# Optimization experiments

Hardware: AMD Instinct MI355X
Metric: run time of the kernel (lower is better)

## Reference

```python
import jax, jax.numpy as jnp
import numpy as np

N_NODES, N_EDGES, MAX_NB = 40000, 80000, 4
INPUT_SIZE, NODE_FDIM, HIDDEN = 384, 256, 256
DEPTH = 6


def setup_inputs() -> dict:
    key = jax.random.key(0)
    ks = jax.random.split(key, 16)
    s = 0.05  # weight init scale
    return {
        "fnode": jax.random.normal(ks[0], (N_NODES, NODE_FDIM), dtype=jnp.float32),
        "fmess": jax.random.normal(ks[1], (N_EDGES, INPUT_SIZE), dtype=jnp.float32),
        "agraph": jax.random.randint(ks[2], (N_NODES, MAX_NB), 0, N_EDGES),
        "bgraph": jax.random.randint(ks[3], (N_EDGES, MAX_NB), 0, N_EDGES),
        "mask": jnp.ones((N_NODES, 1), dtype=jnp.float32),
        "Wz": jax.random.normal(ks[4], (INPUT_SIZE + HIDDEN, HIDDEN), dtype=jnp.float32) * s,
        "bz": jnp.zeros((HIDDEN,), dtype=jnp.float32),
        "Wr": jax.random.normal(ks[5], (INPUT_SIZE, HIDDEN), dtype=jnp.float32) * s,
        "Ur": jax.random.normal(ks[6], (HIDDEN, HIDDEN), dtype=jnp.float32) * s,
        "bur": jnp.zeros((HIDDEN,), dtype=jnp.float32),
        "Wh": jax.random.normal(ks[7], (INPUT_SIZE + HIDDEN, HIDDEN), dtype=jnp.float32) * s,
        "bh": jnp.zeros((HIDDEN,), dtype=jnp.float32),
        "Wo": jax.random.normal(ks[8], (NODE_FDIM + HIDDEN, HIDDEN), dtype=jnp.float32) * s,
        "bo": jnp.zeros((HIDDEN,), dtype=jnp.float32),
        "depth": DEPTH,
    }


def reference(fnode, fmess, agraph, bgraph, mask, Wz, bz, Wr, Ur, bur, Wh, bh, Wo, bo, depth):
    E, H = fmess.shape[0], Wz.shape[1]
    # message 0 is padding -> kept at zero each step (mask[0,0]=0 in torch GRU)
    msg_mask = jnp.ones((E, 1), dtype=fmess.dtype).at[0, 0].set(0.0)
    rx = fmess @ Wr  # precomputable: [E, H], reset gate input term

    def step(h, _):
        h_nei = h[bgraph]                      # [E, nb, H] gather
        sum_h = h_nei.sum(axis=1)              # [E, H]
        z = jax.nn.sigmoid(jnp.concatenate([fmess, sum_h], axis=1) @ Wz + bz)
        r = jax.nn.sigmoid(rx[:, None, :] + h_nei @ Ur + bur)  # [E, nb, H]
        sum_gh = (r * h_nei).sum(axis=1)
        pre_h = jnp.tanh(jnp.concatenate([fmess, sum_gh], axis=1) @ Wh + bh)
        h_new = ((1.0 - z) * sum_h + z * pre_h) * msg_mask
        return h_new, None

    h0 = jnp.zeros((E, H), dtype=fmess.dtype)
    h, _ = jax.lax.scan(step, h0, None, length=depth)

    nei_message = h[agraph].sum(axis=1)        # [N, H] gather-sum over incoming edges
    node_hiddens = jax.nn.relu(jnp.concatenate([fnode, nei_message], axis=1) @ Wo + bo)
    return node_hiddens * mask, h
```

## Files before the change

### kernel.cpp

```cpp
#include <hip/hip_runtime.h>
#include <stdint.h>

#define N_NODES 40000
#define N_EDGES 80000
#define HID 256
#define HC_LD 512
#define DEPTH_FIXED 6
#define NPAD 40064
#define MT 32

typedef __bf16 bf16;
typedef __bf16 bf16x4 __attribute__((ext_vector_type(4)));
typedef __bf16 bf16x8 __attribute__((ext_vector_type(8)));
typedef float f32x4 __attribute__((ext_vector_type(4)));

#define TPAD 136
#define APAD 264

__device__ __forceinline__ float sigmoidf_(float x) { return 1.f / (1.f + __expf(-x)); }
__device__ __forceinline__ float tanhf_(float x) { float e = __expf(2.f * x); return 1.f - 2.f / (e + 1.f); }

__device__ __forceinline__ void gld_lds16(const void* g, void* l) {
    __builtin_amdgcn_global_load_lds(
        (const __attribute__((address_space(1))) uint32_t*)g,
        (__attribute__((address_space(3))) uint32_t*)l, 16, 0, 0);
}

__device__ __forceinline__ void stage_tile(const bf16* __restrict__ src, int ld, int r0, int k0,
                                           bf16* lds, int tid) {
#pragma unroll
    for (int jj = 0; jj < 2; ++jj) {
        int s = jj * 256 + tid;
        int c = s ^ ((s >> 3) & 3);
        gld_lds16(src + (size_t)(r0 + (c >> 2)) * ld + k0 + (c & 3) * 8, lds + s * 8);
    }
}

__device__ __forceinline__ void mfma_tile(const bf16* lds_a, const bf16* lds_b,
                                          int wm, int wn, int lane, f32x4 (&acc)[4][4]) {
    const int li = lane & 15, quad = lane >> 4;
    const int sw = quad ^ ((li >> 1) & 3);
    bf16x8 a[4], b[4];
#pragma unroll
    for (int i = 0; i < 4; ++i)
        a[i] = *(const bf16x8*)(lds_a + ((wm * 64 + i * 16 + li) * 4 + sw) * 8);
#pragma unroll
    for (int j = 0; j < 4; ++j)
        b[j] = *(const bf16x8*)(lds_b + ((wn * 64 + j * 16 + li) * 4 + sw) * 8);
#pragma unroll
    for (int i = 0; i < 4; ++i)
#pragma unroll
        for (int j = 0; j < 4; ++j)
            acc[i][j] = __builtin_amdgcn_mfma_f32_16x16x32_bf16(a[i], b[j], acc[i][j], 0, 0, 0);
}

__global__ __launch_bounds__(256, 3) void step_fused_k(
    const int* __restrict__ bgraph, const bf16* __restrict__ HC,
    const bf16* __restrict__ P,
    const bf16* __restrict__ B1T, const bf16* __restrict__ B2T,
    bf16* __restrict__ HCn, float* __restrict__ HF) {
    __shared__ __align__(16) bf16 sA1[MT * APAD];
    __shared__ __align__(16) bf16 sA2[MT * APAD];
    __shared__ __align__(16) bf16 sBst[256 * 32];
    const int tid = threadIdx.x, lane = tid & 63, wave = tid >> 6;
    const int m0 = blockIdx.x * MT;

    {
        const int r = tid >> 3, qc = tid & 7;
        const int e = m0 + r;
        const int4 nb = *(const int4*)(bgraph + (size_t)e * 4);
        const int bi[4] = {nb.x, nb.y, nb.z, nb.w};
        const bf16* prx = P + (size_t)e * 768 + qc * 32;
        bf16x8 rx[4];
#pragma unroll
        for (int c = 0; c < 4; ++c) rx[c] = *(const bf16x8*)(prx + c * 8);
        float sh[4][8] = {}, gh[4][8] = {};
#pragma unroll
        for (int j = 0; j < 4; ++j) {
            const bf16* hp = HC + (size_t)bi[j] * HC_LD + qc * 32;
            bf16x8 hv[4], uv[4];
#pragma unroll
            for (int c = 0; c < 4; ++c) { hv[c] = *(const bf16x8*)(hp + c * 8); uv[c] = *(const bf16x8*)(hp + 256 + c * 8); }
#pragma unroll
            for (int c = 0; c < 4; ++c)
#pragma unroll
                for (int u = 0; u < 8; ++u) {
                    float hf = (float)hv[c][u];
                    float rr = sigmoidf_((float)rx[c][u] + (float)uv[c][u]);
                    sh[c][u] += hf;
                    gh[c][u] += rr * hf;
                }
        }
#pragma unroll
        for (int c = 0; c < 4; ++c) {
            bf16x8 os, og;
#pragma unroll
            for (int u = 0; u < 8; ++u) { os[u] = (bf16)sh[c][u]; og[u] = (bf16)gh[c][u]; }
            *(bf16x8*)(sA1 + r * APAD + qc * 32 + c * 8) = os;
            *(bf16x8*)(sA2 + r * APAD + qc * 32 + c * 8) = og;
        }
    }
    __syncthreads();

    const int li = lane & 15, quad = lane >> 4;
    const int sw = quad ^ ((li >> 1) & 3);
    f32x4 accZ[2][4] = {}, accH[2][4] = {};
#pragma unroll
    for (int pass = 0; pass < 2; ++pass) {
        const bf16* BT = pass ? B2T : B1T;
        const bf16* sA = pass ? sA2 : sA1;
        for (int t = 0; t < 8; ++t) {
#pragma unroll
            for (int jj = 0; jj < 4; ++jj) {
                int s = jj * 256 + tid;
                int c = s ^ ((s >> 3) & 3);
                gld_lds16(BT + (size_t)(c >> 2) * 256 + t * 32 + (c & 3) * 8, sBst + s * 8);
            }
            __syncthreads();
            bf16x8 a[2], b[4];
#pragma unroll
            for (int i = 0; i < 2; ++i)
                a[i] = *(const bf16x8*)(sA + (i * 16 + li) * APAD + t * 32 + quad * 8);
#pragma unroll
            for (int j = 0; j < 4; ++j)
                b[j] = *(const bf16x8*)(sBst + ((wave * 64 + j * 16 + li) * 4 + sw) * 8);
#pragma unroll
            for (int i = 0; i < 2; ++i)
#pragma unroll
                for (int j = 0; j < 4; ++j) {
                    if (pass == 0) accZ[i][j] = __builtin_amdgcn_mfma_f32_16x16x32_bf16(a[i], b[j], accZ[i][j], 0, 0, 0);
                    else           accH[i][j] = __builtin_amdgcn_mfma_f32_16x16x32_bf16(a[i], b[j], accH[i][j], 0, 0, 0);
                }
            __syncthreads();
        }
    }

    bf16* tZ = sA2;
    bf16* tH = sBst;
#pragma unroll
    for (int i = 0; i < 2; ++i)
#pragma unroll
        for (int j = 0; j < 4; ++j) {
            const int col = wave * 64 + j * 16 + li;
#pragma unroll
            for (int r = 0; r < 4; ++r) {
                const int row = i * 16 + quad * 4 + r;
                tZ[row * APAD + col] = (bf16)accZ[i][j][r];
                tH[row * 256 + col] = (bf16)accH[i][j][r];
            }
        }
    __syncthreads();
#pragma unroll
    for (int s = 0; s < 4; ++s) {
        int v = s * 256 + tid;
        int lr = v >> 5, c8 = (v & 31) * 8;
        int e = m0 + lr;
        bf16x8 zl = *(const bf16x8*)(tZ + lr * APAD + c8);
        bf16x8 hl = *(const bf16x8*)(tH + lr * 256 + c8);
        bf16x8 shv = *(const bf16x8*)(sA1 + lr * APAD + c8);
        bf16x8 zx = *(const bf16x8*)(P + (size_t)e * 768 + 256 + c8);
        bf16x8 hx = *(const bf16x8*)(P + (size_t)e * 768 + 512 + c8);
        bf16x8 o;
        float of[8];
#pragma unroll
        for (int u = 0; u < 8; ++u) {
            float z = sigmoidf_((float)zl[u] + (float)zx[u]);
            float p = tanhf_((float)hl[u] + (float)hx[u]);
            float hn = (1.f - z) * (float)shv[u] + z * p;
            if (e == 0) hn = 0.f;
            o[u] = (bf16)hn;
            of[u] = hn;
        }
        *(bf16x8*)(HCn + (size_t)e * HC_LD + c8) = o;
        if (HF) {
            *(float4*)(HF + (size_t)e * HID + c8) = make_float4(of[0], of[1], of[2], of[3]);
            *(float4*)(HF + (size_t)e * HID + c8 + 4) = make_float4(of[4], of[5], of[6], of[7]);
        }
    }
}

__global__ __launch_bounds__(256) void gemm_single_k(
    const bf16* __restrict__ A, int lda, const bf16* __restrict__ BT,
    const float* __restrict__ bias, bf16* __restrict__ C, int K, int ldc) {
    __shared__ __align__(16) char smem[34816];
    bf16* sA = (bf16*)smem;
    bf16* sB = sA + 4096;
    const int tid = threadIdx.x, lane = tid & 63, wave = tid >> 6;
    const int wm = wave >> 1, wn = wave & 1;
    const int m0 = blockIdx.x * 128, n0 = blockIdx.y * 128;
    f32x4 acc[4][4] = {};
    for (int k0 = 0; k0 < K; k0 += 32) {
        stage_tile(A, lda, m0, k0, sA, tid);
        stage_tile(BT, K, n0, k0, sB, tid);
        __syncthreads();
        mfma_tile(sA, sB, wm, wn, lane, acc);
        __syncthreads();
    }
    bf16* tC = (bf16*)smem;
#pragma unroll
    for (int i = 0; i < 4; ++i)
#pragma unroll
        for (int j = 0; j < 4; ++j) {
            const int col = wn * 64 + j * 16 + (lane & 15);
#pragma unroll
            for (int r = 0; r < 4; ++r) {
                const int lr = wm * 64 + i * 16 + (lane >> 4) * 4 + r;
                tC[lr * TPAD + col] = (bf16)acc[i][j][r];
            }
        }
    __syncthreads();
#pragma unroll
    for (int s = 0; s < 8; ++s) {
        int v = s * 256 + tid;
        int lr = v >> 4, c8 = (v & 15) * 8;
        bf16x8 cv = *(const bf16x8*)(tC + lr * TPAD + c8);
        bf16x8 o;
        if (bias) {
            float4 b0 = *(const float4*)(bias + n0 + c8);
            float4 b1 = *(const float4*)(bias + n0 + c8 + 4);
            o[0] = (bf16)((float)cv[0] + b0.x); o[1] = (bf16)((float)cv[1] + b0.y);
            o[2] = (bf16)((float)cv[2] + b0.z); o[3] = (bf16)((float)cv[3] + b0.w);
            o[4] = (bf16)((float)cv[4] + b1.x); o[5] = (bf16)((float)cv[5] + b1.y);
            o[6] = (bf16)((float)cv[6] + b1.z); o[7] = (bf16)((float)cv[7] + b1.w);
        } else {
            o = cv;
        }
        *(bf16x8*)(C + (size_t)(m0 + lr) * ldc + n0 + c8) = o;
    }
}

__global__ __launch_bounds__(256) void gemm_out_k(
    const bf16* __restrict__ A1, const bf16* __restrict__ A2,
    const bf16* __restrict__ B1T, const bf16* __restrict__ B2T,
    const float* __restrict__ bo, const float* __restrict__ mask, float* __restrict__ out) {
    __shared__ __align__(16) char smem[34816];
    bf16* s0 = (bf16*)smem;
    bf16* s1 = s0 + 4096;
    bf16* s2 = s1 + 4096;
    bf16* s3 = s2 + 4096;
    const int tid = threadIdx.x, lane = tid & 63, wave = tid >> 6;
    const int wm = wave >> 1, wn = wave & 1;
    const int m0 = blockIdx.x * 128, n0 = blockIdx.y * 128;
    f32x4 acc1[4][4] = {}, acc2[4][4] = {};
    for (int k0 = 0; k0 < 256; k0 += 32) {
        stage_tile(A1, 256, m0, k0, s0, tid);
        stage_tile(B1T, 256, n0, k0, s1, tid);
        stage_tile(A2, 256, m0, k0, s2, tid);
        stage_tile(B2T, 256, n0, k0, s3, tid);
        __syncthreads();
        mfma_tile(s0, s1, wm, wn, lane, acc1);
        mfma_tile(s2, s3, wm, wn, lane, acc2);
        __syncthreads();
    }
    bf16* tC = (bf16*)smem;
#pragma unroll
    for (int i = 0; i < 4; ++i)
#pragma unroll
        for (int j = 0; j < 4; ++j) {
            const int col = wn * 64 + j * 16 + (lane & 15);
#pragma unroll
            for (int r = 0; r < 4; ++r) {
                const int lr = wm * 64 + i * 16 + (lane >> 4) * 4 + r;
                tC[lr * TPAD + col] = (bf16)(acc1[i][j][r] + acc2[i][j][r]);
            }
        }
    __syncthreads();
#pragma unroll
    for (int s = 0; s < 8; ++s) {
        int v = s * 256 + tid;
        int lr = v >> 4, c8 = (v & 15) * 8;
        int grow = m0 + lr;
        if (grow >= N_NODES) continue;
        int gcol = n0 + c8;
        bf16x8 cv = *(const bf16x8*)(tC + lr * TPAD + c8);
        float4 b0 = *(const float4*)(bo + gcol);
        float4 b1 = *(const float4*)(bo + gcol + 4);
        float mk = mask[grow];
        float4 o0, o1;
        o0.x = fmaxf((float)cv[0] + b0.x, 0.f) * mk;
        o0.y = fmaxf((float)cv[1] + b0.y, 0.f) * mk;
        o0.z = fmaxf((float)cv[2] + b0.z, 0.f) * mk;
        o0.w = fmaxf((float)cv[3] + b0.w, 0.f) * mk;
        o1.x = fmaxf((float)cv[4] + b1.x, 0.f) * mk;
        o1.y = fmaxf((float)cv[5] + b1.y, 0.f) * mk;
        o1.z = fmaxf((float)cv[6] + b1.z, 0.f) * mk;
        o1.w = fmaxf((float)cv[7] + b1.w, 0.f) * mk;
        *(float4*)(out + (size_t)grow * 256 + gcol) = o0;
        *(float4*)(out + (size_t)grow * 256 + gcol + 4) = o1;
    }
}

__global__ __launch_bounds__(256) void gather_nei_k(
    const int* __restrict__ agraph, const bf16* __restrict__ H, bf16* __restrict__ nei) {
    int i = blockIdx.x * 256 + threadIdx.x;
    int v = i >> 5, c8 = (i & 31) * 8;
    bf16x8 o;
    if (v < N_NODES) {
        int4 nb = *(const int4*)(agraph + (size_t)v * 4);
        int bi[4] = {nb.x, nb.y, nb.z, nb.w};
        float s[8] = {};
#pragma unroll
        for (int j = 0; j < 4; ++j) {
            bf16x8 hv = *(const bf16x8*)(H + (size_t)bi[j] * HC_LD + c8);
#pragma unroll
            for (int r = 0; r < 8; ++r) s[r] += (float)hv[r];
        }
#pragma unroll
        for (int r = 0; r < 8; ++r) o[r] = (bf16)s[r];
    } else {
#pragma unroll
        for (int r = 0; r < 8; ++r) o[r] = (bf16)0.f;
    }
    *(bf16x8*)(nei + (size_t)v * HID + c8) = o;
}

__global__ __launch_bounds__(256) void step1_k(const bf16* __restrict__ P, bf16* __restrict__ HC) {
    int i = blockIdx.x * 256 + threadIdx.x;
    int e = i >> 5, c8 = (i & 31) * 8;
    bf16x8 zx = *(const bf16x8*)(P + (size_t)e * 768 + 256 + c8);
    bf16x8 hx = *(const bf16x8*)(P + (size_t)e * 768 + 512 + c8);
    bf16x8 o;
#pragma unroll
    for (int r = 0; r < 8; ++r) {
        float h = sigmoidf_((float)zx[r]) * tanhf_((float)hx[r]);
        if (e == 0) h = 0.f;
        o[r] = (bf16)h;
    }
    *(bf16x8*)(HC + (size_t)e * HC_LD + c8) = o;
}

__global__ void cvt_bf16_k(const float* __restrict__ src, bf16* __restrict__ dst, int n4) {
    int i = blockIdx.x * 256 + threadIdx.x;
    if (i >= n4) return;
    float4 v = ((const float4*)src)[i];
    bf16x4 o = {(bf16)v.x, (bf16)v.y, (bf16)v.z, (bf16)v.w};
    *((bf16x4*)dst + i) = o;
}

__global__ void cvt_fnode_k(const float* __restrict__ src, bf16* __restrict__ dst) {
    int i = blockIdx.x * 256 + threadIdx.x;
    int row = i >> 6;
    bf16x4 o = {(bf16)0.f, (bf16)0.f, (bf16)0.f, (bf16)0.f};
    if (row < N_NODES) {
        float4 v = ((const float4*)src)[i];
        o[0] = (bf16)v.x; o[1] = (bf16)v.y; o[2] = (bf16)v.z; o[3] = (bf16)v.w;
    }
    *((bf16x4*)dst + i) = o;
}

__global__ void prep_wpre_k(const float* __restrict__ Wr, const float* __restrict__ Wz,
                            const float* __restrict__ Wh, bf16* __restrict__ WT) {
    int idx = blockIdx.x * 256 + threadIdx.x;
    if (idx >= 768 * 384) return;
    int n = idx / 384, k = idx % 384;
    float v;
    if (n < 256) v = Wr[(size_t)k * 256 + n];
    else if (n < 512) v = Wz[(size_t)k * 256 + (n - 256)];
    else v = Wh[(size_t)k * 256 + (n - 512)];
    WT[idx] = (bf16)v;
}

__global__ void prep_bias_k(const float* __restrict__ bur, const float* __restrict__ bz,
                            const float* __restrict__ bh, float* __restrict__ bp) {
    int n = blockIdx.x * 256 + threadIdx.x;
    if (n >= 768) return;
    bp[n] = n < 256 ? bur[n] : (n < 512 ? bz[n - 256] : bh[n - 512]);
}

__global__ void prep_t256_k(const float* __restrict__ W, bf16* __restrict__ T, int roff) {
    int idx = blockIdx.x * 256 + threadIdx.x;
    int n = idx >> 8, k = idx & 255;
    T[idx] = (bf16)W[(size_t)(roff + k) * 256 + n];
}

extern "C" void kernel_launch(void* const* d_in, const int* in_sizes, int n_in,
                              void* d_out, int out_size, void* d_ws, size_t ws_size,
                              hipStream_t stream) {
    (void)in_sizes; (void)n_in; (void)out_size; (void)ws_size;
    const float* fnode = (const float*)d_in[0];
    const float* fmess = (const float*)d_in[1];
    const int* agraph = (const int*)d_in[2];
    const int* bgraph = (const int*)d_in[3];
    const float* mask = (const float*)d_in[4];
    const float* Wz = (const float*)d_in[5];
    const float* bz = (const float*)d_in[6];
    const float* Wr = (const float*)d_in[7];
    const float* Ur = (const float*)d_in[8];
    const float* bur = (const float*)d_in[9];
    const float* Wh = (const float*)d_in[10];
    const float* bh = (const float*)d_in[11];
    const float* Wo = (const float*)d_in[12];
    const float* bo = (const float*)d_in[13];
    float* out_node = (float*)d_out;
    float* out_h = out_node + (size_t)N_NODES * HID;

    char* ws = (char*)d_ws;
    size_t off = 0;
    auto alloc = [&](size_t b) -> char* { char* p = ws + off; off += (b + 255) & ~(size_t)255; return p; };
    bf16* P     = (bf16*)alloc((size_t)N_EDGES * 768 * 2);
    bf16* HC0   = (bf16*)alloc((size_t)N_EDGES * HC_LD * 2);
    bf16* HC1   = (bf16*)alloc((size_t)N_EDGES * HC_LD * 2);
    bf16* fnodeB= (bf16*)alloc((size_t)NPAD * HID * 2);
    bf16* nei   = (bf16*)alloc((size_t)NPAD * HID * 2);
    bf16* WTpre = (bf16*)alloc((size_t)768 * 384 * 2);
    bf16* UrT   = (bf16*)alloc(65536 * 2);
    bf16* WzBT  = (bf16*)alloc(65536 * 2);
    bf16* WhBT  = (bf16*)alloc(65536 * 2);
    bf16* WoTT  = (bf16*)alloc(65536 * 2);
    bf16* WoBT  = (bf16*)alloc(65536 * 2);
    float* biasP= (float*)alloc(768 * 4);
    bf16* fmessB = HC1;

    cvt_bf16_k<<<30000, 256, 0, stream>>>(fmess, fmessB, N_EDGES * 384 / 4);
    cvt_fnode_k<<<NPAD * 64 / 256, 256, 0, stream>>>(fnode, fnodeB);
    prep_wpre_k<<<(768 * 384 + 255) / 256, 256, 0, stream>>>(Wr, Wz, Wh, WTpre);
    prep_bias_k<<<3, 256, 0, stream>>>(bur, bz, bh, biasP);
    prep_t256_k<<<256, 256, 0, stream>>>(Ur, UrT, 0);
    prep_t256_k<<<256, 256, 0, stream>>>(Wz, WzBT, 384);
    prep_t256_k<<<256, 256, 0, stream>>>(Wh, WhBT, 384);
    prep_t256_k<<<256, 256, 0, stream>>>(Wo, WoTT, 0);
    prep_t256_k<<<256, 256, 0, stream>>>(Wo, WoBT, 256);

    gemm_single_k<<<dim3(625, 6), 256, 0, stream>>>(fmessB, 384, WTpre, biasP, P, 384, 768);

    step1_k<<<N_EDGES * 32 / 256, 256, 0, stream>>>(P, HC0);

    bf16* cur = HC0;
    bf16* nxt = HC1;
    for (int d = 2; d <= DEPTH_FIXED; ++d) {
        gemm_single_k<<<dim3(625, 2), 256, 0, stream>>>(cur, HC_LD, UrT, nullptr, cur + 256, 256, HC_LD);
        step_fused_k<<<N_EDGES / MT, 256, 0, stream>>>(bgraph, cur, P, WzBT, WhBT, nxt,
                                                       d == DEPTH_FIXED ? out_h : nullptr);
        bf16* t = cur; cur = nxt; nxt = t;
    }

    gather_nei_k<<<NPAD * 32 / 256, 256, 0, stream>>>(agraph, cur, nei);
    gemm_out_k<<<dim3(313, 2), 256, 0, stream>>>(fnodeB, nei, WoTT, WoBT, bo, mask, out_node);
}
```

Before: 1.399 ms.

## Halve edge tile and prefetch per-wave weight slices without block barriers

Shrinks the fused GRU step tile from 32 to 16 edges per block, doubling the block count, and raises the occupancy hint to 4 blocks. Each wave now loads only its own slice of the weight tile into LDS and issues the next k-slice's loads before the current MFMAs, replacing the two per-iteration block barriers with wait counters. The gather phase is re-split so 16 threads cover one edge row. This aims to raise parallelism and hide weight-load latency. The cost is reloading each weight matrix for twice as many blocks, and MFMA work per weight load drops by half.

After: 1.252 ms. 1.12x faster.

```diff
diff --git a/kernel.cpp b/kernel.cpp
--- a/kernel.cpp
+++ b/kernel.cpp
@@ -7,7 +7,7 @@
 #define HC_LD 512
 #define DEPTH_FIXED 6
 #define NPAD 40064
-#define MT 32
+#define MT 16
 
 typedef __bf16 bf16;
 typedef __bf16 bf16x4 __attribute__((ext_vector_type(4)));
@@ -54,7 +54,7 @@
             acc[i][j] = __builtin_amdgcn_mfma_f32_16x16x32_bf16(a[i], b[j], acc[i][j], 0, 0, 0);
 }
 
-__global__ __launch_bounds__(256, 3) void step_fused_k(
+__global__ __launch_bounds__(256, 4) void step_fused_k(
     const int* __restrict__ bgraph, const bf16* __restrict__ HC,
     const bf16* __restrict__ P,
     const bf16* __restrict__ B1T, const bf16* __restrict__ B2T,
@@ -64,94 +64,111 @@
     __shared__ __align__(16) bf16 sBst[256 * 32];
     const int tid = threadIdx.x, lane = tid & 63, wave = tid >> 6;
     const int m0 = blockIdx.x * MT;
+    const int li = lane & 15, quad = lane >> 4;
+
+#pragma unroll
+    for (int jj = 0; jj < 4; ++jj) {
+        int s = wave * 256 + jj * 64 + lane;
+        int c = s ^ ((s >> 3) & 3);
+        gld_lds16(B1T + (size_t)(c >> 2) * 256 + (c & 3) * 8, sBst + s * 8);
+    }
 
     {
-        const int r = tid >> 3, qc = tid & 7;
+        const int r = tid >> 4, qc = tid & 15;
         const int e = m0 + r;
         const int4 nb = *(const int4*)(bgraph + (size_t)e * 4);
         const int bi[4] = {nb.x, nb.y, nb.z, nb.w};
-        const bf16* prx = P + (size_t)e * 768 + qc * 32;
-        bf16x8 rx[4];
-#pragma unroll
-        for (int c = 0; c < 4; ++c) rx[c] = *(const bf16x8*)(prx + c * 8);
-        float sh[4][8] = {}, gh[4][8] = {};
-#pragma unroll
-        for (int j = 0; j < 4; ++j) {
-            const bf16* hp = HC + (size_t)bi[j] * HC_LD + qc * 32;
-            bf16x8 hv[4], uv[4];
-#pragma unroll
-            for (int c = 0; c < 4; ++c) { hv[c] = *(const bf16x8*)(hp + c * 8); uv[c] = *(const bf16x8*)(hp + 256 + c * 8); }
-#pragma unroll
-            for (int c = 0; c < 4; ++c)
-#pragma unroll
-                for (int u = 0; u < 8; ++u) {
-                    float hf = (float)hv[c][u];
-                    float rr = sigmoidf_((float)rx[c][u] + (float)uv[c][u]);
-                    sh[c][u] += hf;
-                    gh[c][u] += rr * hf;
-                }
-        }
-#pragma unroll
-        for (int c = 0; c < 4; ++c) {
+        const bf16* prx = P + (size_t)e * 768 + qc * 16;
+        bf16x8 rx[2];
+        rx[0] = *(const bf16x8*)(prx);
+        rx[1] = *(const bf16x8*)(prx + 8);
+        float sh[2][8] = {}, gh[2][8] = {};
+#pragma unroll
+        for (int p = 0; p < 2; ++p) {
+            bf16x8 hv[2][2], uv[2][2];
+#pragma unroll
+            for (int jj = 0; jj < 2; ++jj) {
+                const bf16* hp = HC + (size_t)bi[p * 2 + jj] * HC_LD + qc * 16;
+                hv[jj][0] = *(const bf16x8*)(hp);
+                hv[jj][1] = *(const bf16x8*)(hp + 8);
+                uv[jj][0] = *(const bf16x8*)(hp + 256);
+                uv[jj][1] = *(const bf16x8*)(hp + 256 + 8);
+            }
+#pragma unroll
+            for (int jj = 0; jj < 2; ++jj)
+#pragma unroll
+                for (int c = 0; c < 2; ++c)
+#pragma unroll
+                    for (int u = 0; u < 8; ++u) {
+                        float hf = (float)hv[jj][c][u];
+                        float rr = sigmoidf_((float)rx[c][u] + (float)uv[jj][c][u]);
+                        sh[c][u] += hf;
+                        gh[c][u] += rr * hf;
+                    }
+        }
+#pragma unroll
+        for (int c = 0; c < 2; ++c) {
             bf16x8 os, og;
 #pragma unroll
             for (int u = 0; u < 8; ++u) { os[u] = (bf16)sh[c][u]; og[u] = (bf16)gh[c][u]; }
-            *(bf16x8*)(sA1 + r * APAD + qc * 32 + c * 8) = os;
-            *(bf16x8*)(sA2 + r * APAD + qc * 32 + c * 8) = og;
+            *(bf16x8*)(sA1 + r * APAD + qc * 16 + c * 8) = os;
+            *(bf16x8*)(sA2 + r * APAD + qc * 16 + c * 8) = og;
         }
     }
     __syncthreads();
 
-    const int li = lane & 15, quad = lane >> 4;
     const int sw = quad ^ ((li >> 1) & 3);
-    f32x4 accZ[2][4] = {}, accH[2][4] = {};
+    f32x4 accZ[4] = {}, accH[4] = {};
 #pragma unroll
     for (int pass = 0; pass < 2; ++pass) {
-        const bf16* BT = pass ? B2T : B1T;
         const bf16* sA = pass ? sA2 : sA1;
+#pragma unroll
         for (int t = 0; t < 8; ++t) {
-#pragma unroll
-            for (int jj = 0; jj < 4; ++jj) {
-                int s = jj * 256 + tid;
-                int c = s ^ ((s >> 3) & 3);
-                gld_lds16(BT + (size_t)(c >> 2) * 256 + t * 32 + (c & 3) * 8, sBst + s * 8);
-            }
-            __syncthreads();
-            bf16x8 a[2], b[4];
-#pragma unroll
-            for (int i = 0; i < 2; ++i)
-                a[i] = *(const bf16x8*)(sA + (i * 16 + li) * APAD + t * 32 + quad * 8);
+            asm volatile("s_waitcnt vmcnt(0)" ::: "memory");
+            __builtin_amdgcn_sched_barrier(0);
+            bf16x8 a = *(const bf16x8*)(sA + li * APAD + t * 32 + quad * 8);
+            bf16x8 b[4];
 #pragma unroll
             for (int j = 0; j < 4; ++j)
                 b[j] = *(const bf16x8*)(sBst + ((wave * 64 + j * 16 + li) * 4 + sw) * 8);
-#pragma unroll
-            for (int i = 0; i < 2; ++i)
-#pragma unroll
-                for (int j = 0; j < 4; ++j) {
-                    if (pass == 0) accZ[i][j] = __builtin_amdgcn_mfma_f32_16x16x32_bf16(a[i], b[j], accZ[i][j], 0, 0, 0);
-                    else           accH[i][j] = __builtin_amdgcn_mfma_f32_16x16x32_bf16(a[i], b[j], accH[i][j], 0, 0, 0);
+            asm volatile("s_waitcnt lgkmcnt(0)" ::: "memory");
+            __builtin_amdgcn_sched_barrier(0);
+            const int un = pass * 8 + t + 1;
+            if (un < 16) {
+                const bf16* BTn = (un < 8) ? B1T : B2T;
+                const int tn = un & 7;
+#pragma unroll
+                for (int jj = 0; jj < 4; ++jj) {
+                    int s = wave * 256 + jj * 64 + lane;
+                    int c = s ^ ((s >> 3) & 3);
+                    gld_lds16(BTn + (size_t)(c >> 2) * 256 + tn * 32 + (c & 3) * 8, sBst + s * 8);
                 }
-            __syncthreads();
-        }
-    }
+            }
+#pragma unroll
+            for (int j = 0; j < 4; ++j) {
+                if (pass == 0) accZ[j] = __builtin_amdgcn_mfma_f32_16x16x32_bf16(a, b[j], accZ[j], 0, 0, 0);
+                else           accH[j] = __builtin_amdgcn_mfma_f32_16x16x32_bf16(a, b[j], accH[j], 0, 0, 0);
+            }
+        }
+    }
+
+    __syncthreads();
 
     bf16* tZ = sA2;
     bf16* tH = sBst;
 #pragma unroll
-    for (int i = 0; i < 2; ++i)
-#pragma unroll
-        for (int j = 0; j < 4; ++j) {
-            const int col = wave * 64 + j * 16 + li;
-#pragma unroll
-            for (int r = 0; r < 4; ++r) {
-                const int row = i * 16 + quad * 4 + r;
-                tZ[row * APAD + col] = (bf16)accZ[i][j][r];
-                tH[row * 256 + col] = (bf16)accH[i][j][r];
-            }
-        }
+    for (int j = 0; j < 4; ++j) {
+        const int col = wave * 64 + j * 16 + li;
+#pragma unroll
+        for (int r = 0; r < 4; ++r) {
+            const int row = quad * 4 + r;
+            tZ[row * APAD + col] = (bf16)accZ[j][r];
+            tH[row * 256 + col] = (bf16)accH[j][r];
+        }
+    }
     __syncthreads();
 #pragma unroll
-    for (int s = 0; s < 4; ++s) {
+    for (int s = 0; s < 2; ++s) {
         int v = s * 256 + tid;
         int lr = v >> 5, c8 = (v & 31) * 8;
         int e = m0 + lr;
```
